# Kernel tuning notes

Hardware: AMD Instinct MI355X
Metric: run time of the kernel (lower is better)

Reference implementation:

```python
import jax, jax.numpy as jnp
import numpy as np

N_STEPS = 3  # fixed propagation depth standing in for the BFS-guided delta_st recursion


def setup_inputs() -> dict:
    key = jax.random.key(0)
    ks = jax.random.split(key, 12)
    n, d, E = 32, 96, 256
    f32 = jnp.float32
    rn = lambda k, s, sc: jax.random.normal(k, s, f32) * sc
    return {
        "node_embeddings": rn(ks[0], (n, d), 1.0),
        "edges": jax.random.randint(ks[1], (E, 2), 0, n, jnp.int32),
        "w1": rn(ks[2], (4, 4, 3), 0.3), "b1": jnp.full((4,), 0.01, f32),
        "w2": rn(ks[3], (4, 4, 3), 0.3), "b2": jnp.full((4,), 0.01, f32),
        "w3": rn(ks[4], (4, 4, 3), 0.3), "b3": jnp.full((4,), 0.01, f32),
        "fc1_w": rn(ks[5], (16, 128), 0.2), "fc1_b": jnp.full((128,), 0.01, f32),
        "fc2_w": rn(ks[6], (128, 256), 0.1), "fc2_b": jnp.full((256,), 0.01, f32),
        "fc3_w": rn(ks[7], (256, 128), 0.1), "fc3_b": jnp.full((128,), 0.01, f32),
        "fc4_w": rn(ks[8], (128, 1), 0.1), "fc4_b": jnp.full((1,), 0.01, f32),
    }


def _conv1d(x, w, b, stride):
    # x: [B, C, L], w: [O, I, K]
    y = jax.lax.conv_general_dilated(x, w, (stride,), 'VALID',
                                     dimension_numbers=('NCH', 'OIH', 'NCH'))
    return y + b[None, :, None]


def _maxpool2(x):
    return jax.lax.reduce_window(x, -jnp.inf, jax.lax.max, (1, 1, 2), (1, 1, 2), 'VALID')


def _conv_pool_stack(x, w1, b1, w2, b2, w3, b3,
                     fc1_w, fc1_b, fc2_w, fc2_b, fc3_w, fc3_b, fc4_w, fc4_b):
    # x: [B, 4, 96] -> [B]
    h = _maxpool2(jax.nn.relu(_conv1d(x, w1, b1, 2)))   # [B,4,23]
    h = _maxpool2(jax.nn.relu(_conv1d(h, w2, b2, 1)))   # [B,4,10]
    h = _maxpool2(jax.nn.relu(_conv1d(h, w3, b3, 1)))   # [B,4,4]
    h = h.reshape(h.shape[0], -1)                       # [B,16]
    h = jax.nn.relu(h @ fc1_w + fc1_b)
    h = jax.nn.relu(h @ fc2_w + fc2_b)
    h = jax.nn.relu(h @ fc3_w + fc3_b)
    return (h @ fc4_w + fc4_b)[:, 0]


def reference(node_embeddings, edges, w1, b1, w2, b2, w3, b3,
              fc1_w, fc1_b, fc2_w, fc2_b, fc3_w, fc3_b, fc4_w, fc4_b):
    n, d = node_embeddings.shape
    E = edges.shape[0]
    u_idx, v_idx = edges[:, 0], edges[:, 1]

    # All (s, t) node pairs, flattened: P = n*n (s == t masked out below).
    s_idx, t_idx = jnp.meshgrid(jnp.arange(n), jnp.arange(n), indexing='ij')
    s_idx, t_idx = s_idx.reshape(-1), t_idx.reshape(-1)
    P = n * n

    se = node_embeddings[s_idx]  # [P, d]
    te = node_embeddings[t_idx]  # [P, d]
    ue = node_embeddings[u_idx]  # [E, d]
    ve = node_embeddings[v_idx]  # [E, d]

    # stuv input: [P, E, 4, d] -> [P*E, 4, d]
    stuv = jnp.stack([
        jnp.broadcast_to(se[:, None, :], (P, E, d)),
        jnp.broadcast_to(te[:, None, :], (P, E, d)),
        jnp.broadcast_to(ue[None, :, :], (P, E, d)),
        jnp.broadcast_to(ve[None, :, :], (P, E, d)),
    ], axis=2).reshape(P * E, 4, d)

    preds = _conv_pool_stack(stuv, w1, b1, w2, b2, w3, b3,
                             fc1_w, fc1_b, fc2_w, fc2_b,
                             fc3_w, fc3_b, fc4_w, fc4_b).reshape(P, E)

    # zero out s == t pairs (the original skips them)
    preds = preds * (s_idx != t_idx).astype(preds.dtype)[:, None]

    # delta_st: propagate unit mass from s through the per-pair sparse routing
    # matrix R[u, v] = preds[p, e] for N_STEPS hops, accumulating arrivals.
    x = jax.nn.one_hot(s_idx, n, dtype=preds.dtype)  # [P, n]
    rbc = jnp.zeros((n,), preds.dtype)
    for _ in range(N_STEPS):
        gathered = x[:, u_idx] * preds                      # [P, E]
        x = jnp.zeros((P, n), preds.dtype).at[:, v_idx].add(gathered)
        rbc = rbc + x.sum(axis=0)

    return rbc / jnp.sum(rbc)
```

## Files before the change

kernel.cpp:

```cpp
#include <hip/hip_runtime.h>

constexpr int F_ELEMS = 4 * 32 * 4 * 48;
constexpr int PREDS_OFF = F_ELEMS;
constexpr int RBCP_OFF = PREDS_OFF + 1024 * 256;
constexpr int CNT_OFF = RBCP_OFF + 2048;
constexpr int W1P_OFF = CNT_OFF + 16;
constexpr int W2P_OFF = W1P_OFF + 2048;
constexpr int W3P_OFF = W2P_OFF + 16384;

typedef __attribute__((ext_vector_type(8))) short short8;
typedef __attribute__((ext_vector_type(4))) short short4v;
typedef __attribute__((ext_vector_type(4))) float f32x4;
typedef __attribute__((ext_vector_type(2))) unsigned int uint2v;

__device__ __forceinline__ unsigned short f2bf(float x) {
    unsigned u = __float_as_uint(x);
    u += 0x7FFF + ((u >> 16) & 1);
    return (unsigned short)(u >> 16);
}

__device__ __forceinline__ unsigned cvt_pk_bf16(float a, float b) {
    unsigned r;
    asm("v_cvt_pk_bf16_f32 %0, %1, %2" : "=v"(r) : "v"(a), "v"(b));
    return r;
}

template <int CTRL>
__device__ __forceinline__ float qp(float x) {
    return __int_as_float(__builtin_amdgcn_update_dpp(
        0, __float_as_int(x), CTRL, 0xF, 0xF, true));
}

__global__ void prep_all(const float* __restrict__ emb, const float* __restrict__ w1,
                         const float* __restrict__ fc1_w, const float* __restrict__ fc2_w,
                         const float* __restrict__ fc3_w,
                         float* __restrict__ F, unsigned short* __restrict__ W1p,
                         unsigned short* __restrict__ W2p, unsigned short* __restrict__ W3p,
                         float* __restrict__ rbcp_zero) {
    int b = blockIdx.x;
    if (b < 96) {
        int idx = b * 256 + threadIdx.x;
        int i = idx % 48;
        int o = (idx / 48) % 4;
        int node = (idx / 192) % 32;
        int c = idx / 6144;
        float acc = 0.f;
        if (i < 46) {
#pragma unroll
            for (int k = 0; k < 3; k++) acc += w1[(o * 4 + c) * 3 + k] * emb[node * 96 + 2 * i + k];
        }
        F[idx] = acc;
        return;
    }
    if (b < 112) {
        int t = (b - 96) * 256 + threadIdx.x;
        int j = t & 7, lane = (t >> 3) & 63, mt = t >> 9;
        int k = (lane >> 4) * 8 + j, n = mt * 16 + (lane & 15);
        float w = (k < 16) ? fc1_w[k * 128 + n] : 0.f;
        W1p[t] = f2bf(w);
        return;
    }
    if (b < 240) {
        int t = (b - 112) * 256 + threadIdx.x;
        int j = t & 7, lane = (t >> 3) & 63, ks = (t >> 9) & 3, mt = t >> 11;
        int k = ks * 32 + (lane >> 4) * 8 + j, n = mt * 16 + (lane & 15);
        W2p[t] = f2bf(fc2_w[k * 256 + n]);
        return;
    }
    if (b < 368) {
        int t = (b - 240) * 256 + threadIdx.x;
        int j = t & 7, lane = (t >> 3) & 63, ks = (t >> 9) & 7, mt = t >> 12;
        int k = ks * 32 + (lane >> 4) * 8 + j, n = mt * 16 + (lane & 15);
        W3p[t] = f2bf(fc3_w[k * 128 + n]);
        return;
    }
    for (int k = threadIdx.x; k < 2064; k += 256) rbcp_zero[k] = 0.f;
}

__global__ __launch_bounds__(256, 4)
void mlp_kernel(const float* __restrict__ F, const int* __restrict__ edges,
                const float* __restrict__ b1v,
                const float* __restrict__ w2, const float* __restrict__ b2,
                const float* __restrict__ w3, const float* __restrict__ b3,
                const float* __restrict__ fc1_b, const float* __restrict__ fc2_b,
                const float* __restrict__ fc3_b,
                const float* __restrict__ fc4_w, const float* __restrict__ fc4_b,
                const unsigned short* __restrict__ W1p, const unsigned short* __restrict__ W2p,
                const unsigned short* __restrict__ W3p,
                float* __restrict__ preds) {
    __shared__ __align__(16) float smem[8448];
    unsigned short* X1 = (unsigned short*)smem;
    unsigned short* X3h = (unsigned short*)smem;
    unsigned short* X2 = (unsigned short*)(smem + 4096);
    float* part = smem + 8192;

    const int tid = threadIdx.x;
    const int p = blockIdx.x >> 2;
    const int e0 = (blockIdx.x & 3) * 64;
    const int s = p >> 5, t = p & 31;
    if (s == t) return;

    const int lane = tid & 63, wave = tid >> 6;
    const int mrow = lane & 15, quad = lane >> 4;

    const int gsample = tid >> 2, o = tid & 3;
    float h1[23];
    {
        const int e = e0 + gsample;
        const int u = edges[2 * e], v = edges[2 * e + 1];
        const f32x4* F0 = (const f32x4*)(F + ((0 * 32 + s) * 4 + o) * 48);
        const f32x4* F1 = (const f32x4*)(F + ((1 * 32 + t) * 4 + o) * 48);
        const f32x4* F2 = (const f32x4*)(F + ((2 * 32 + u) * 4 + o) * 48);
        const f32x4* F3 = (const f32x4*)(F + ((3 * 32 + v) * 4 + o) * 48);
        const float bb = b1v[o];
        float pre[46];
#pragma unroll
        for (int q = 0; q < 12; q++) {
            f32x4 x = F0[q] + F1[q] + F2[q] + F3[q];
#pragma unroll
            for (int z = 0; z < 4; z++) {
                int i = 4 * q + z;
                if (i < 46) pre[i] = x[z] + bb;
            }
        }
#pragma unroll
        for (int j = 0; j < 23; j++) h1[j] = fmaxf(fmaxf(pre[2 * j], pre[2 * j + 1]), 0.f);
    }
    float h2[10];
    {
        float wm[4][3];
#pragma unroll
        for (int m = 0; m < 4; m++)
#pragma unroll
            for (int k = 0; k < 3; k++) wm[m][k] = w2[o * 12 + (o ^ m) * 3 + k];
        const float bb = b2[o];
        float win[4][3];
#pragma unroll
        for (int j = 0; j < 2; j++) {
            float x = h1[j];
            win[0][j] = x;
            win[1][j] = qp<0xB1>(x);
            win[2][j] = qp<0x4E>(x);
            win[3][j] = qp<0x1B>(x);
        }
        float pre[20];
#pragma unroll
        for (int i = 0; i < 20; i++) {
            float x = h1[i + 2];
            win[0][(i + 2) % 3] = x;
            win[1][(i + 2) % 3] = qp<0xB1>(x);
            win[2][(i + 2) % 3] = qp<0x4E>(x);
            win[3][(i + 2) % 3] = qp<0x1B>(x);
            float acc = bb;
#pragma unroll
            for (int m = 0; m < 4; m++)
#pragma unroll
                for (int k = 0; k < 3; k++)
                    acc = fmaf(wm[m][k], win[m][(i + k) % 3], acc);
            pre[i] = acc;
        }
#pragma unroll
        for (int j = 0; j < 10; j++) h2[j] = fmaxf(fmaxf(pre[2 * j], pre[2 * j + 1]), 0.f);
    }
    {
        float wm[4][3];
#pragma unroll
        for (int m = 0; m < 4; m++)
#pragma unroll
            for (int k = 0; k < 3; k++) wm[m][k] = w3[o * 12 + (o ^ m) * 3 + k];
        const float bb = b3[o];
        float win[4][3];
#pragma unroll
        for (int j = 0; j < 2; j++) {
            float x = h2[j];
            win[0][j] = x;
            win[1][j] = qp<0xB1>(x);
            win[2][j] = qp<0x4E>(x);
            win[3][j] = qp<0x1B>(x);
        }
        float pre[8];
#pragma unroll
        for (int i = 0; i < 8; i++) {
            float x = h2[i + 2];
            win[0][(i + 2) % 3] = x;
            win[1][(i + 2) % 3] = qp<0xB1>(x);
            win[2][(i + 2) % 3] = qp<0x4E>(x);
            win[3][(i + 2) % 3] = qp<0x1B>(x);
            float acc = bb;
#pragma unroll
            for (int m = 0; m < 4; m++)
#pragma unroll
                for (int k = 0; k < 3; k++)
                    acc = fmaf(wm[m][k], win[m][(i + k) % 3], acc);
            pre[i] = acc;
        }
        float v0 = fmaxf(fmaxf(pre[0], pre[1]), 0.f);
        float v1 = fmaxf(fmaxf(pre[2], pre[3]), 0.f);
        float v2 = fmaxf(fmaxf(pre[4], pre[5]), 0.f);
        float v3 = fmaxf(fmaxf(pre[6], pre[7]), 0.f);
        uint2v d;
        d.x = cvt_pk_bf16(v0, v1);
        d.y = cvt_pk_bf16(v2, v3);
        *(uint2v*)(X1 + (((o >> 1) * 64 + gsample) * 8) + (o & 1) * 4) = d;
        uint2v z2 = (uint2v){0u, 0u};
        *(uint2v*)(X1 + ((((o >> 1) + 2) * 64 + gsample) * 8) + (o & 1) * 4) = z2;
    }
    const short8* W1v = (const short8*)W1p;
    short8 w1f[2];
#pragma unroll
    for (int mtl = 0; mtl < 2; mtl++)
        w1f[mtl] = W1v[(wave * 2 + mtl) * 64 + lane];
    __syncthreads();
    {
        short8 bnt[4];
#pragma unroll
        for (int nt = 0; nt < 4; nt++)
            bnt[nt] = *(const short8*)(X1 + (quad * 64 + nt * 16 + mrow) * 8);
        f32x4 acc1[2][4];
#pragma unroll
        for (int a = 0; a < 2; a++)
#pragma unroll
            for (int b = 0; b < 4; b++) acc1[a][b] = (f32x4){0.f, 0.f, 0.f, 0.f};
#pragma unroll
        for (int mtl = 0; mtl < 2; mtl++) {
#pragma unroll
            for (int nt = 0; nt < 4; nt++)
                acc1[mtl][nt] = __builtin_amdgcn_mfma_f32_16x16x32_bf16(w1f[mtl], bnt[nt], acc1[mtl][nt], 0, 0, 0);
        }
#pragma unroll
        for (int mtl = 0; mtl < 2; mtl++) {
            const int mt = wave * 2 + mtl;
            const int n0 = mt * 16 + quad * 4;
            f32x4 b4 = *(const f32x4*)(fc1_b + n0);
#pragma unroll
            for (int nt = 0; nt < 4; nt++) {
                float x0 = fmaxf(acc1[mtl][nt][0] + b4[0], 0.f);
                float x1 = fmaxf(acc1[mtl][nt][1] + b4[1], 0.f);
                float x2 = fmaxf(acc1[mtl][nt][2] + b4[2], 0.f);
                float x3 = fmaxf(acc1[mtl][nt][3] + b4[3], 0.f);
                uint2v d;
                d.x = cvt_pk_bf16(x0, x1);
                d.y = cvt_pk_bf16(x2, x3);
                *(uint2v*)(X2 + ((n0 >> 3) * 64 + nt * 16 + mrow) * 8 + (n0 & 7)) = d;
            }
        }
    }
    __syncthreads();
    const short8* W2v = (const short8*)W2p;
    const short8* W3v = (const short8*)W3p;
    f32x4 acc3[2][4];
#pragma unroll
    for (int a = 0; a < 2; a++)
#pragma unroll
        for (int b = 0; b < 4; b++) acc3[a][b] = (f32x4){0.f, 0.f, 0.f, 0.f};
#pragma unroll
    for (int h = 0; h < 2; h++) {
        short8 w2f[2][4];
#pragma unroll
        for (int mtl = 0; mtl < 2; mtl++)
#pragma unroll
            for (int ks = 0; ks < 4; ks++)
                w2f[mtl][ks] = W2v[((h * 8 + wave * 2 + mtl) * 4 + ks) * 64 + lane];
        f32x4 acc2[2][4];
#pragma unroll
        for (int a = 0; a < 2; a++)
#pragma unroll
            for (int b = 0; b < 4; b++) acc2[a][b] = (f32x4){0.f, 0.f, 0.f, 0.f};
#pragma unroll
        for (int ks = 0; ks < 4; ks++) {
            short8 bfr[4];
#pragma unroll
            for (int nt = 0; nt < 4; nt++)
                bfr[nt] = *(const short8*)(X2 + ((ks * 4 + quad) * 64 + nt * 16 + mrow) * 8);
#pragma unroll
            for (int mtl = 0; mtl < 2; mtl++) {
#pragma unroll
                for (int nt = 0; nt < 4; nt++)
                    acc2[mtl][nt] = __builtin_amdgcn_mfma_f32_16x16x32_bf16(w2f[mtl][ks], bfr[nt], acc2[mtl][nt], 0, 0, 0);
            }
        }
        short8 w3f[2][4];
#pragma unroll
        for (int mtl = 0; mtl < 2; mtl++)
#pragma unroll
            for (int ksl = 0; ksl < 4; ksl++)
                w3f[mtl][ksl] = W3v[((wave * 2 + mtl) * 8 + h * 4 + ksl) * 64 + lane];
#pragma unroll
        for (int mtl = 0; mtl < 2; mtl++) {
            const int mt = h * 8 + wave * 2 + mtl;
            const int n0 = mt * 16 + quad * 4;
            const int kl = n0 - h * 128;
            f32x4 b4 = *(const f32x4*)(fc2_b + n0);
#pragma unroll
            for (int nt = 0; nt < 4; nt++) {
                float x0 = fmaxf(acc2[mtl][nt][0] + b4[0], 0.f);
                float x1 = fmaxf(acc2[mtl][nt][1] + b4[1], 0.f);
                float x2 = fmaxf(acc2[mtl][nt][2] + b4[2], 0.f);
                float x3 = fmaxf(acc2[mtl][nt][3] + b4[3], 0.f);
                uint2v d;
                d.x = cvt_pk_bf16(x0, x1);
                d.y = cvt_pk_bf16(x2, x3);
                *(uint2v*)(X3h + ((kl >> 3) * 64 + nt * 16 + mrow) * 8 + (kl & 7)) = d;
            }
        }
        __syncthreads();
#pragma unroll
        for (int ksl = 0; ksl < 4; ksl++) {
            short8 bfr[4];
#pragma unroll
            for (int nt = 0; nt < 4; nt++)
                bfr[nt] = *(const short8*)(X3h + ((ksl * 4 + quad) * 64 + nt * 16 + mrow) * 8);
#pragma unroll
            for (int mtl = 0; mtl < 2; mtl++) {
#pragma unroll
                for (int nt = 0; nt < 4; nt++)
                    acc3[mtl][nt] = __builtin_amdgcn_mfma_f32_16x16x32_bf16(w3f[mtl][ksl], bfr[nt], acc3[mtl][nt], 0, 0, 0);
            }
        }
        __syncthreads();
    }
    {
        float p4[4] = {0.f, 0.f, 0.f, 0.f};
#pragma unroll
        for (int mtl = 0; mtl < 2; mtl++) {
            const int mt = wave * 2 + mtl;
            const int n0 = mt * 16 + quad * 4;
            f32x4 b4 = *(const f32x4*)(fc3_b + n0);
            f32x4 w44 = *(const f32x4*)(fc4_w + n0);
#pragma unroll
            for (int nt = 0; nt < 4; nt++)
#pragma unroll
                for (int r = 0; r < 4; r++)
                    p4[nt] = fmaf(fmaxf(acc3[mtl][nt][r] + b4[r], 0.f), w44[r], p4[nt]);
        }
#pragma unroll
        for (int nt = 0; nt < 4; nt++) {
            p4[nt] += __shfl_xor(p4[nt], 16, 64);
            p4[nt] += __shfl_xor(p4[nt], 32, 64);
        }
        if (quad == 0) {
#pragma unroll
            for (int nt = 0; nt < 4; nt++)
                part[wave * 64 + nt * 16 + mrow] = p4[nt];
        }
    }
    __syncthreads();
    if (tid < 64) {
        float pred = part[tid] + part[64 + tid] + part[128 + tid] + part[192 + tid] + fc4_b[0];
        preds[p * 256 + e0 + tid] = pred;
    }
}

__global__ __launch_bounds__(256)
void prop_kernel(const int* __restrict__ edges, const float* __restrict__ preds,
                 float* __restrict__ rbc_part) {
    const int tid = threadIdx.x;
    const int wave = tid >> 6, lane = tid & 63;
    const int p = blockIdx.x * 4 + wave;
    const int s = p >> 5, t = p & 31;
    __shared__ float xw[4][32], xnw[4][32], raccw[4][32];
    int u[4], v[4];
    float pr[4];
#pragma unroll
    for (int j = 0; j < 4; j++) {
        int e = lane + 64 * j;
        u[j] = edges[2 * e];
        v[j] = edges[2 * e + 1];
        pr[j] = preds[p * 256 + e];
    }
    if (lane < 32) { xw[wave][lane] = (lane == s) ? 1.f : 0.f; raccw[wave][lane] = 0.f; }
    const bool active = (s != t);
    for (int step = 0; step < 3; step++) {
        if (lane < 32) xnw[wave][lane] = 0.f;
        __syncthreads();
        if (active) {
#pragma unroll
            for (int j = 0; j < 4; j++)
                atomicAdd(&xnw[wave][v[j]], xw[wave][u[j]] * pr[j]);
        }
        __syncthreads();
        if (lane < 32) { raccw[wave][lane] += xnw[wave][lane]; xw[wave][lane] = xnw[wave][lane]; }
        __syncthreads();
    }
    if (active && lane < 32) atomicAdd(&rbc_part[(p & 63) * 32 + lane], raccw[wave][lane]);
}

__global__ __launch_bounds__(256)
void norm_kernel(const float* __restrict__ rbc_part, float* __restrict__ out) {
    const int tid = threadIdx.x;
    const int node = tid & 31, sub = tid >> 5;
    __shared__ float red[8][32];
    float vv = 0.f;
#pragma unroll
    for (int g = 0; g < 8; g++)
        vv += rbc_part[(sub * 8 + g) * 32 + node];
    red[sub][node] = vv;
    __syncthreads();
    if (tid < 32) {
        float acc = 0.f;
#pragma unroll
        for (int sb = 0; sb < 8; sb++) acc += red[sb][tid];
        float tot = acc;
#pragma unroll
        for (int mask = 1; mask < 32; mask <<= 1) tot += __shfl_xor(tot, mask, 32);
        out[tid] = acc / tot;
    }
}

extern "C" void kernel_launch(void* const* d_in, const int* in_sizes, int n_in,
                              void* d_out, int out_size, void* d_ws, size_t ws_size,
                              hipStream_t stream) {
    const float* emb = (const float*)d_in[0];
    const int* edges = (const int*)d_in[1];
    const float* w1 = (const float*)d_in[2];
    const float* b1 = (const float*)d_in[3];
    const float* w2 = (const float*)d_in[4];
    const float* b2 = (const float*)d_in[5];
    const float* w3 = (const float*)d_in[6];
    const float* b3 = (const float*)d_in[7];
    const float* fc1_w = (const float*)d_in[8];
    const float* fc1_b = (const float*)d_in[9];
    const float* fc2_w = (const float*)d_in[10];
    const float* fc2_b = (const float*)d_in[11];
    const float* fc3_w = (const float*)d_in[12];
    const float* fc3_b = (const float*)d_in[13];
    const float* fc4_w = (const float*)d_in[14];
    const float* fc4_b = (const float*)d_in[15];

    float* ws = (float*)d_ws;
    float* F = ws;
    float* preds = ws + PREDS_OFF;
    float* rbc_part = ws + RBCP_OFF;
    unsigned short* W1p = (unsigned short*)(ws + W1P_OFF);
    unsigned short* W2p = (unsigned short*)(ws + W2P_OFF);
    unsigned short* W3p = (unsigned short*)(ws + W3P_OFF);
    float* out = (float*)d_out;

    prep_all<<<dim3(369), dim3(256), 0, stream>>>(emb, w1, fc1_w, fc2_w, fc3_w,
                                                  F, W1p, W2p, W3p, rbc_part);
    mlp_kernel<<<dim3(4096), dim3(256), 0, stream>>>(
        F, edges, b1, w2, b2, w3, b3, fc1_b, fc2_b, fc3_b,
        fc4_w, fc4_b, W1p, W2p, W3p, preds);
    prop_kernel<<<dim3(256), dim3(256), 0, stream>>>(edges, preds, rbc_part);
    norm_kernel<<<dim3(1), dim3(256), 0, stream>>>(rbc_part, out);
}
```

Before: 165.5 us.

## Compute full fc2 output at once, then run fc3 over full K

Replaces the two-half interleaved fc2/fc3 loop with a single fc2 pass that computes all 256 outputs per block into 16 accumulator tiles, writes the whole activation to shared memory, then runs fc3 over K=256 in one loop. Weight fragments are now loaded per k-step inside the loop instead of prefetched into register arrays. This cuts one pair of barriers and the split schedule but doubles the live fc2 accumulator count, raising register pressure under the 256x4 launch bound and possibly causing spills or lower occupancy.

```diff
diff --git a/kernel.cpp b/kernel.cpp
--- a/kernel.cpp
+++ b/kernel.cpp
@@ -90,7 +90,7 @@
                 float* __restrict__ preds) {
     __shared__ __align__(16) float smem[8448];
     unsigned short* X1 = (unsigned short*)smem;
-    unsigned short* X3h = (unsigned short*)smem;
+    unsigned short* X3f = (unsigned short*)smem;
     unsigned short* X2 = (unsigned short*)(smem + 4096);
     float* part = smem + 8192;
 
@@ -248,76 +248,64 @@
     __syncthreads();
     const short8* W2v = (const short8*)W2p;
     const short8* W3v = (const short8*)W3p;
+    f32x4 acc2[4][4];
+#pragma unroll
+    for (int a = 0; a < 4; a++)
+#pragma unroll
+        for (int b = 0; b < 4; b++) acc2[a][b] = (f32x4){0.f, 0.f, 0.f, 0.f};
+#pragma unroll
+    for (int ks = 0; ks < 4; ks++) {
+        short8 bfr[4];
+#pragma unroll
+        for (int nt = 0; nt < 4; nt++)
+            bfr[nt] = *(const short8*)(X2 + ((ks * 4 + quad) * 64 + nt * 16 + mrow) * 8);
+#pragma unroll
+        for (int q = 0; q < 4; q++) {
+            const int mt = q * 4 + wave;
+            short8 ah = W2v[(mt * 4 + ks) * 64 + lane];
+#pragma unroll
+            for (int nt = 0; nt < 4; nt++)
+                acc2[q][nt] = __builtin_amdgcn_mfma_f32_16x16x32_bf16(ah, bfr[nt], acc2[q][nt], 0, 0, 0);
+        }
+    }
+    __syncthreads();
+#pragma unroll
+    for (int q = 0; q < 4; q++) {
+        const int mt = q * 4 + wave;
+        const int n0 = mt * 16 + quad * 4;
+        f32x4 b4 = *(const f32x4*)(fc2_b + n0);
+#pragma unroll
+        for (int nt = 0; nt < 4; nt++) {
+            float x0 = fmaxf(acc2[q][nt][0] + b4[0], 0.f);
+            float x1 = fmaxf(acc2[q][nt][1] + b4[1], 0.f);
+            float x2 = fmaxf(acc2[q][nt][2] + b4[2], 0.f);
+            float x3 = fmaxf(acc2[q][nt][3] + b4[3], 0.f);
+            uint2v d;
+            d.x = cvt_pk_bf16(x0, x1);
+            d.y = cvt_pk_bf16(x2, x3);
+            *(uint2v*)(X3f + ((n0 >> 3) * 64 + nt * 16 + mrow) * 8 + (n0 & 7)) = d;
+        }
+    }
+    __syncthreads();
     f32x4 acc3[2][4];
 #pragma unroll
     for (int a = 0; a < 2; a++)
 #pragma unroll
         for (int b = 0; b < 4; b++) acc3[a][b] = (f32x4){0.f, 0.f, 0.f, 0.f};
 #pragma unroll
-    for (int h = 0; h < 2; h++) {
-        short8 w2f[2][4];
-#pragma unroll
-        for (int mtl = 0; mtl < 2; mtl++)
-#pragma unroll
-            for (int ks = 0; ks < 4; ks++)
-                w2f[mtl][ks] = W2v[((h * 8 + wave * 2 + mtl) * 4 + ks) * 64 + lane];
-        f32x4 acc2[2][4];
-#pragma unroll
-        for (int a = 0; a < 2; a++)
-#pragma unroll
-            for (int b = 0; b < 4; b++) acc2[a][b] = (f32x4){0.f, 0.f, 0.f, 0.f};
-#pragma unroll
-        for (int ks = 0; ks < 4; ks++) {
-            short8 bfr[4];
+    for (int ks = 0; ks < 8; ks++) {
+        short8 bfr[4];
+#pragma unroll
+        for (int nt = 0; nt < 4; nt++)
+            bfr[nt] = *(const short8*)(X3f + ((ks * 4 + quad) * 64 + nt * 16 + mrow) * 8);
+#pragma unroll
+        for (int mtl = 0; mtl < 2; mtl++) {
+            const int mt = wave * 2 + mtl;
+            short8 ah = W3v[(mt * 8 + ks) * 64 + lane];
 #pragma unroll
             for (int nt = 0; nt < 4; nt++)
-                bfr[nt] = *(const short8*)(X2 + ((ks * 4 + quad) * 64 + nt * 16 + mrow) * 8);
-#pragma unroll
-            for (int mtl = 0; mtl < 2; mtl++) {
-#pragma unroll
-                for (int nt = 0; nt < 4; nt++)
-                    acc2[mtl][nt] = __builtin_amdgcn_mfma_f32_16x16x32_bf16(w2f[mtl][ks], bfr[nt], acc2[mtl][nt], 0, 0, 0);
-            }
-        }
-        short8 w3f[2][4];
-#pragma unroll
-        for (int mtl = 0; mtl < 2; mtl++)
-#pragma unroll
-            for (int ksl = 0; ksl < 4; ksl++)
-                w3f[mtl][ksl] = W3v[((wave * 2 + mtl) * 8 + h * 4 + ksl) * 64 + lane];
-#pragma unroll
-        for (int mtl = 0; mtl < 2; mtl++) {
-            const int mt = h * 8 + wave * 2 + mtl;
-            const int n0 = mt * 16 + quad * 4;
-            const int kl = n0 - h * 128;
-            f32x4 b4 = *(const f32x4*)(fc2_b + n0);
-#pragma unroll
-            for (int nt = 0; nt < 4; nt++) {
-                float x0 = fmaxf(acc2[mtl][nt][0] + b4[0], 0.f);
-                float x1 = fmaxf(acc2[mtl][nt][1] + b4[1], 0.f);
-                float x2 = fmaxf(acc2[mtl][nt][2] + b4[2], 0.f);
-                float x3 = fmaxf(acc2[mtl][nt][3] + b4[3], 0.f);
-                uint2v d;
-                d.x = cvt_pk_bf16(x0, x1);
-                d.y = cvt_pk_bf16(x2, x3);
-                *(uint2v*)(X3h + ((kl >> 3) * 64 + nt * 16 + mrow) * 8 + (kl & 7)) = d;
-            }
-        }
-        __syncthreads();
-#pragma unroll
-        for (int ksl = 0; ksl < 4; ksl++) {
-            short8 bfr[4];
-#pragma unroll
-            for (int nt = 0; nt < 4; nt++)
-                bfr[nt] = *(const short8*)(X3h + ((ksl * 4 + quad) * 64 + nt * 16 + mrow) * 8);
-#pragma unroll
-            for (int mtl = 0; mtl < 2; mtl++) {
-#pragma unroll
-                for (int nt = 0; nt < 4; nt++)
-                    acc3[mtl][nt] = __builtin_amdgcn_mfma_f32_16x16x32_bf16(w3f[mtl][ksl], bfr[nt], acc3[mtl][nt], 0, 0, 0);
-            }
-        }
-        __syncthreads();
+                acc3[mtl][nt] = __builtin_amdgcn_mfma_f32_16x16x32_bf16(ah, bfr[nt], acc3[mtl][nt], 0, 0, 0);
+        }
     }
     {
         float p4[4] = {0.f, 0.f, 0.f, 0.f};
```

After: 163.2 us. Within noise of the previous version (-1.4%).
